# Kernel optimization log

Measured on AMD Instinct MI355X. Metric: run time of the kernel, lower is better.

Reference implementation:

```python
import jax, jax.numpy as jnp
import numpy as np

B, N, F = 1024, 256, 8
E = 1024
OUT = 128          # NNConv out-channels (hardcoded in module)
N_DIV = 64         # len(num_actions)
PER = 3            # actions per diverter
FEAT = N * OUT     # feature_size() = num_nodes * 128


def setup_inputs() -> dict:
    key = jax.random.key(0)
    ks = jax.random.split(key, 20)
    s = lambda *sh: 0.02
    return {
        "x": jax.random.normal(ks[0], (B, N, F), jnp.float32),
        "edge_index": jax.random.randint(ks[1], (2, E), 0, N, jnp.int64),
        # edge-MLP nn1: Linear(1,64) -> ReLU -> Linear(64, F*OUT)
        "w1": jax.random.normal(ks[2], (1, 64), jnp.float32) * 0.1,
        "b1": jnp.zeros((64,), jnp.float32),
        "w2": jax.random.normal(ks[3], (64, F * OUT), jnp.float32) * 0.02,
        "b2": jnp.zeros((F * OUT,), jnp.float32),
        # NNConv root weight + bias
        "root_w": jax.random.normal(ks[4], (F, OUT), jnp.float32) * 0.1,
        "conv_b": jnp.zeros((OUT,), jnp.float32),
        # dueling heads
        "adv_w": jax.random.normal(ks[5], (FEAT, N_DIV * PER), jnp.float32) * 0.005,
        "adv_b": jnp.zeros((N_DIV * PER,), jnp.float32),
        "v1w": jax.random.normal(ks[6], (FEAT, 64), jnp.float32) * 0.005,
        "v1b": jnp.zeros((64,), jnp.float32),
        "v2w": jax.random.normal(ks[7], (64, 64), jnp.float32) * 0.1,
        "v2b": jnp.zeros((64,), jnp.float32),
        "v3w": jax.random.normal(ks[8], (64, N_DIV), jnp.float32) * 0.1,
        "v3b": jnp.zeros((N_DIV,), jnp.float32),
    }


def reference(x, edge_index, w1, b1, w2, b2, root_w, conv_b,
              adv_w, adv_b, v1w, v1b, v2w, v2b, v3w, v3b):
    b, n, f = x.shape
    out_c = root_w.shape[1]
    n_div = v3w.shape[1]
    flat = x.reshape(b * n, f)                              # [B*N, F]
    e = edge_index.shape[1]
    # edge_attr = ones -> edge MLP produces per-edge weight matrix theta
    ea = jnp.ones((e, 1), x.dtype)
    h = jax.nn.relu(ea @ w1 + b1)
    theta = (h @ w2 + b2).reshape(e, f, out_c)              # [E, F, OUT]
    src, tgt = edge_index[0], edge_index[1]
    # gather source feats -> per-edge matmul -> scatter-add at targets
    msg = jnp.einsum('ef,efo->eo', flat[src], theta)        # [E, OUT]
    agg = jnp.zeros((b * n, out_c), x.dtype).at[tgt].add(msg)
    conv = agg + flat @ root_w + conv_b                      # NNConv root + bias
    feat = jax.nn.relu(conv).reshape(b, -1)                  # [B, N*OUT]
    adv = jax.nn.relu(feat @ adv_w + adv_b).reshape(b, n_div, -1)
    val = jax.nn.relu(feat @ v1w + v1b)
    val = jax.nn.relu(val @ v2w + v2b)
    val = val @ v3w + v3b                                    # [B, n_div]
    return val[..., None] + adv - adv.mean(-1, keepdims=True)
```

## Files before the change

kernel.cpp:

```cpp
#include <hip/hip_runtime.h>

#define Bsz 1024
#define Nn 256
#define Fdim 8
#define Eedge 1024
#define OUTC 128
#define CADV 192
#define CTOT 256
#define Ktot 32768
#define ASTR 40
#define XSTR 24

typedef __attribute__((ext_vector_type(8))) short short8;
typedef __attribute__((ext_vector_type(4))) float float4v;

static __device__ inline unsigned short f2bf(float f) {
  union { float f; unsigned u; } v; v.f = f;
  unsigned r = v.u + 0x7FFFu + ((v.u >> 16) & 1u);
  return (unsigned short)(r >> 16);
}
static __device__ inline float bf2f(unsigned short h) {
  union { unsigned u; float f; } v; v.u = ((unsigned)h) << 16;
  return v.f;
}
static __device__ inline uint4 pack8(const unsigned short* b) {
  uint4 v;
  v.x = (unsigned)b[0] | ((unsigned)b[1] << 16);
  v.y = (unsigned)b[2] | ((unsigned)b[3] << 16);
  v.z = (unsigned)b[4] | ((unsigned)b[5] << 16);
  v.w = (unsigned)b[6] | ((unsigned)b[7] << 16);
  return v;
}

__global__ __launch_bounds__(256) void prep_feat_kernel(
    const float* __restrict__ x, const int* __restrict__ ei,
    const float* __restrict__ w1, const float* __restrict__ b1,
    const float* __restrict__ w2, const float* __restrict__ b2,
    const float* __restrict__ rootw, const float* __restrict__ convb,
    const float* __restrict__ advw, const float* __restrict__ v1w,
    unsigned short* __restrict__ wt, unsigned short* __restrict__ feat0)
{
  __shared__ __align__(16) char smem[20480];
  int bid = blockIdx.x, t = threadIdx.x;

  if (bid < 16) {
    float* fs   = (float*)smem;
    float* h_s  = fs;
    float* rw_s = fs + 64;
    float* th_s = fs + 128;
    float* pt_s = fs + 192;
    float* S_s  = fs + 448;
    int*   flag = (int*)(fs + 2496);
    int obase = bid * 8;

    if (t < 64) {
      h_s[t]  = fmaxf(w1[t] + b1[t], 0.f);
      rw_s[t] = rootw[(t >> 3) * OUTC + obase + (t & 7)];
    }
    for (int i = t; i < Nn * Fdim; i += 256) S_s[i] = 0.f;
    if (t == 0) {
      int z = 0;
      for (int i = 1; i < 16; i += 2) z |= ei[i];
      *flag = (z == 0);
    }
    __syncthreads();
    int is64 = *flag;

    {
      int l = t & 63, g = t >> 6;
      int c = (l >> 3) * 128 + obase + (l & 7);
      float p = 0.f;
#pragma unroll
      for (int j = 0; j < 16; ++j)
        p += h_s[g * 16 + j] * w2[(size_t)(g * 16 + j) * 1024 + c];
      pt_s[t] = p;
    }
    int srcs[4], tgts[4];
#pragma unroll
    for (int q = 0; q < 4; ++q) {
      int e = t + q * 256;
      if (is64) { srcs[q] = ei[2 * e]; tgts[q] = ei[2 * (Eedge + e)]; }
      else      { srcs[q] = ei[e];     tgts[q] = ei[Eedge + e]; }
      srcs[q] &= 255; tgts[q] &= 255;
    }
    __syncthreads();
    if (t < 64) {
      int c = (t >> 3) * 128 + obase + (t & 7);
      th_s[t] = b2[c] + pt_s[t] + pt_s[t + 64] + pt_s[t + 128] + pt_s[t + 192];
    }
#pragma unroll
    for (int q = 0; q < 4; ++q) {
      const float* xp = x + srcs[q] * Fdim;
#pragma unroll
      for (int f = 0; f < Fdim; ++f)
        atomicAdd(&S_s[tgts[q] * Fdim + f], xp[f]);
    }
    __syncthreads();
    {
      int n = t;
      const float* xp = x + n * Fdim;
      float4 xa = *(const float4*)xp;
      float4 xb = *(const float4*)(xp + 4);
      float xv[8] = {xa.x, xa.y, xa.z, xa.w, xb.x, xb.y, xb.z, xb.w};
      float sv[8];
#pragma unroll
      for (int f = 0; f < 8; ++f) sv[f] = S_s[n * Fdim + f];
      unsigned short buf[8];
#pragma unroll
      for (int oi = 0; oi < 8; ++oi) {
        float z = convb[obase + oi];
#pragma unroll
        for (int f = 0; f < 8; ++f)
          z += xv[f] * rw_s[f * 8 + oi] + sv[f] * th_s[f * 8 + oi];
        buf[oi] = f2bf(fmaxf(z, 0.f));
      }
      *(uint4*)(feat0 + (size_t)n * OUTC + obase) = pack8(buf);
    }
  } else {
    unsigned short* st = (unsigned short*)smem;
    int kt = bid - 16, c = t;
    const float* src; int stride, col;
    if (c < CADV) { src = advw; stride = CADV; col = c; }
    else          { src = v1w;  stride = 64;   col = c - CADV; }
    float v[32];
#pragma unroll
    for (int i = 0; i < 32; ++i)
      v[i] = src[(size_t)(kt * 32 + i) * stride + col];
    unsigned short bv[32];
#pragma unroll
    for (int i = 0; i < 32; ++i) bv[i] = f2bf(v[i]);
#pragma unroll
    for (int p = 0; p < 4; ++p)
      *(uint4*)(st + c * ASTR + p * 8) = pack8(bv + p * 8);
    __syncthreads();
    uint4* dst = (uint4*)(wt + (size_t)kt * (CTOT * 32));
    for (int r = 0; r < 4; ++r) {
      int s = r * 256 + c;
      dst[s] = *(const uint4*)(st + (s >> 2) * ASTR + (s & 3) * 8);
    }
  }
}

__global__ __launch_bounds__(512, 2) void gemm_mfma(
    const float* __restrict__ x, const unsigned short* __restrict__ wt,
    const float* __restrict__ rootw, const float* __restrict__ convb,
    const unsigned short* __restrict__ feat0, float* __restrict__ part,
    int iters, int ns)
{
  __shared__ short a_s[2][128 * ASTR];
  __shared__ short b_s[2][256 * ASTR];
  __shared__ short x_s[2][128 * XSTR];
  __shared__ short rw_s[128 * XSTR];
  __shared__ float convb_s[128];
  int t = threadIdx.x;
  int ch = blockIdx.x;
  int mb = blockIdx.y;
  int wave = t >> 6, lane = t & 63;
  int wm = wave >> 2, wn = wave & 3;
  int lm = lane & 15, lq = lane >> 4;

  float4v acc[4][4];
#pragma unroll
  for (int i = 0; i < 4; ++i)
#pragma unroll
    for (int j = 0; j < 4; ++j) acc[i][j] = (float4v)0.f;

  int kt0 = ch * iters;
  int iters4 = iters >> 2;
  int n0 = ch * iters4;
  int wr0 = (t >> 2) * ASTR + (t & 3) * 8;
  int u1 = t + 512;
  int wr1 = (u1 >> 2) * ASTR + (u1 & 3) * 8;

  if (t < 128) {
    float wv[8];
#pragma unroll
    for (int f = 0; f < 8; ++f) wv[f] = rootw[f * OUTC + t];
    unsigned short wh[8], wl[8];
#pragma unroll
    for (int f = 0; f < 8; ++f) {
      wh[f] = f2bf(wv[f]);
      wl[f] = f2bf(wv[f] - bf2f(wh[f]));
    }
    *(uint4*)(rw_s + t * XSTR)     = pack8(wh);
    *(uint4*)(rw_s + t * XSTR + 8) = pack8(wl);
    convb_s[t] = convb[t];
  }
  int xr = (t & 255) >> 1, xh = t & 1;
  const float* xgb = x + ((size_t)(mb * 128 + xr) * Nn) * Fdim + xh * 4;
  if (t < 256) {
    float4 xv = *(const float4*)(xgb + (size_t)n0 * Fdim);
    float xa[4] = {xv.x, xv.y, xv.z, xv.w};
    unsigned short hh[4], ll[4];
#pragma unroll
    for (int f = 0; f < 4; ++f) {
      hh[f] = f2bf(xa[f]);
      ll[f] = f2bf(xa[f] - bf2f(hh[f]));
    }
    uint2 dh, dl;
    dh.x = (unsigned)hh[0] | ((unsigned)hh[1] << 16);
    dh.y = (unsigned)hh[2] | ((unsigned)hh[3] << 16);
    dl.x = (unsigned)ll[0] | ((unsigned)ll[1] << 16);
    dl.y = (unsigned)ll[2] | ((unsigned)ll[3] << 16);
    *(uint2*)(x_s[0] + xr * XSTR + xh * 4)     = dh;
    *(uint2*)(x_s[0] + xr * XSTR + 8 + xh * 4) = dl;
  }
  __syncthreads();

  {
    int bloc = wave * 16 + lm;
    short8 xf = (short8)0;
    if (lq == 0 || lq == 2) xf = *(const short8*)(x_s[0] + bloc * XSTR);
    else if (lq == 1)       xf = *(const short8*)(x_s[0] + bloc * XSTR + 8);
#pragma unroll
    for (int tt = 0; tt < 2; ++tt) {
      int ot = tt;
      short8 wf = (short8)0;
      if (lq <= 1)      wf = *(const short8*)(rw_s + (ot * 16 + lm) * XSTR);
      else if (lq == 2) wf = *(const short8*)(rw_s + (ot * 16 + lm) * XSTR + 8);
      float4v c = __builtin_amdgcn_mfma_f32_16x16x32_bf16(wf, xf, (float4v)0.f, 0, 0, 0);
      int o0 = ot * 16 + lq * 4;
      float4 cb = *(const float4*)(convb_s + o0);
      unsigned d0 = (unsigned)f2bf(fmaxf(c[0] + cb.x, 0.f)) |
                    ((unsigned)f2bf(fmaxf(c[1] + cb.y, 0.f)) << 16);
      unsigned d1 = (unsigned)f2bf(fmaxf(c[2] + cb.z, 0.f)) |
                    ((unsigned)f2bf(fmaxf(c[3] + cb.w, 0.f)) << 16);
      if (mb == 0 && bloc == 0) {
        const unsigned* f0p = (const unsigned*)(feat0 + ((size_t)n0 * OUTC + o0));
        d0 = f0p[0]; d1 = f0p[1];
      }
      uint2 dd; dd.x = d0; dd.y = d1;
      *(uint2*)(a_s[0] + bloc * ASTR + tt * 16 + lq * 4) = dd;
    }
  }

  const uint4* gB = (const uint4*)wt + (size_t)kt0 * 1024;
  uint4 vb0 = gB[t], vb1 = gB[t + 512];
  float4 xpf = {0.f, 0.f, 0.f, 0.f};

  for (int kk = 0; kk < iters; ++kk) {
    int g = kk & 3, grp = kk >> 2;
    short* bb = b_s[kk & 1];
    *(uint4*)(bb + wr0) = vb0;
    *(uint4*)(bb + wr1) = vb1;
    if (g == 0 && grp + 1 < iters4 && t < 256)
      xpf = *(const float4*)(xgb + (size_t)(n0 + grp + 1) * Fdim);
    if (g == 3 && grp + 1 < iters4 && t < 256) {
      float xa[4] = {xpf.x, xpf.y, xpf.z, xpf.w};
      unsigned short hh[4], ll[4];
#pragma unroll
      for (int f = 0; f < 4; ++f) {
        hh[f] = f2bf(xa[f]);
        ll[f] = f2bf(xa[f] - bf2f(hh[f]));
      }
      uint2 dh, dl;
      dh.x = (unsigned)hh[0] | ((unsigned)hh[1] << 16);
      dh.y = (unsigned)hh[2] | ((unsigned)hh[3] << 16);
      dl.x = (unsigned)ll[0] | ((unsigned)ll[1] << 16);
      dl.y = (unsigned)ll[2] | ((unsigned)ll[3] << 16);
      short* xd = x_s[(grp + 1) & 1];
      *(uint2*)(xd + xr * XSTR + xh * 4)     = dh;
      *(uint2*)(xd + xr * XSTR + 8 + xh * 4) = dl;
    }
    if (kk + 1 < iters) {
      const uint4* gB2 = (const uint4*)wt + (size_t)(kt0 + kk + 1) * 1024;
      vb0 = gB2[t]; vb1 = gB2[t + 512];
    }
    __syncthreads();

    short* ab = a_s[kk & 1];
    short8 aF[4];
#pragma unroll
    for (int i = 0; i < 4; ++i)
      aF[i] = *(const short8*)(ab + (wm * 64 + i * 16 + lm) * ASTR + lq * 8);
#pragma unroll
    for (int j = 0; j < 4; ++j) {
      short8 bF = *(const short8*)(bb + (wn * 64 + j * 16 + lm) * ASTR + lq * 8);
#pragma unroll
      for (int i = 0; i < 4; ++i)
        acc[i][j] = __builtin_amdgcn_mfma_f32_16x16x32_bf16(bF, aF[i], acc[i][j], 0, 0, 0);
    }

    if (kk + 1 < iters) {
      int kn = kk + 1;
      int g2 = kn & 3, grp2 = kn >> 2;
      const short* xs = x_s[grp2 & 1];
      int node2 = n0 + grp2;
      short* ad = a_s[kn & 1];
      int bloc = wave * 16 + lm;
      short8 xf = (short8)0;
      if (lq == 0 || lq == 2) xf = *(const short8*)(xs + bloc * XSTR);
      else if (lq == 1)       xf = *(const short8*)(xs + bloc * XSTR + 8);
#pragma unroll
      for (int tt = 0; tt < 2; ++tt) {
        int ot = g2 * 2 + tt;
        short8 wf = (short8)0;
        if (lq <= 1)      wf = *(const short8*)(rw_s + (ot * 16 + lm) * XSTR);
        else if (lq == 2) wf = *(const short8*)(rw_s + (ot * 16 + lm) * XSTR + 8);
        float4v c = __builtin_amdgcn_mfma_f32_16x16x32_bf16(wf, xf, (float4v)0.f, 0, 0, 0);
        int o0 = ot * 16 + lq * 4;
        float4 cb = *(const float4*)(convb_s + o0);
        unsigned d0 = (unsigned)f2bf(fmaxf(c[0] + cb.x, 0.f)) |
                      ((unsigned)f2bf(fmaxf(c[1] + cb.y, 0.f)) << 16);
        unsigned d1 = (unsigned)f2bf(fmaxf(c[2] + cb.z, 0.f)) |
                      ((unsigned)f2bf(fmaxf(c[3] + cb.w, 0.f)) << 16);
        if (mb == 0 && bloc == 0) {
          const unsigned* f0p = (const unsigned*)(feat0 + ((size_t)node2 * OUTC + o0));
          d0 = f0p[0]; d1 = f0p[1];
        }
        uint2 dd; dd.x = d0; dd.y = d1;
        *(uint2*)(ad + bloc * ASTR + tt * 16 + lq * 4) = dd;
      }
    }
  }

  float* pb = part + ((size_t)(mb * 128) * ns + ch) * CTOT;
#pragma unroll
  for (int i = 0; i < 4; ++i) {
    int m = wm * 64 + i * 16 + lm;
#pragma unroll
    for (int j = 0; j < 4; ++j) {
      int c = wn * 64 + j * 16 + lq * 4;
      *(float4v*)(pb + (size_t)m * ns * CTOT + c) = acc[i][j];
    }
  }
}

__global__ __launch_bounds__(256) void final_kernel(
    const float* __restrict__ part, int ns,
    const float* __restrict__ advb, const float* __restrict__ v1b,
    const float* __restrict__ v2w, const float* __restrict__ v2b,
    const float* __restrict__ v3w, const float* __restrict__ v3b,
    float* __restrict__ out)
{
  __shared__ float adv_s[CADV];
  __shared__ float v1_s[64];
  __shared__ float val2_s[64];
  __shared__ float val3_s[64];
  int b = blockIdx.x, t = threadIdx.x;
  float s = 0.f;
  const float* p = part + (size_t)b * ns * CTOT + t;
  for (int i = 0; i < ns; ++i) s += p[(size_t)i * CTOT];
  if (t < CADV) adv_s[t] = fmaxf(s + advb[t], 0.f);
  else          v1_s[t - CADV] = fmaxf(s + v1b[t - CADV], 0.f);
  __syncthreads();
  if (t < 64) {
    float a = v2b[t];
#pragma unroll
    for (int i = 0; i < 64; ++i) a += v1_s[i] * v2w[i * 64 + t];
    val2_s[t] = fmaxf(a, 0.f);
  }
  __syncthreads();
  if (t < 64) {
    float a = v3b[t];
#pragma unroll
    for (int j = 0; j < 64; ++j) a += val2_s[j] * v3w[j * 64 + t];
    val3_s[t] = a;
  }
  __syncthreads();
  if (t < CADV) {
    int d = t / 3;
    float mean = (adv_s[d * 3] + adv_s[d * 3 + 1] + adv_s[d * 3 + 2]) * (1.f / 3.f);
    out[(size_t)b * CADV + t] = val3_s[d] + adv_s[t] - mean;
  }
}

extern "C" void kernel_launch(void* const* d_in, const int* in_sizes, int n_in,
                              void* d_out, int out_size, void* d_ws, size_t ws_size,
                              hipStream_t stream)
{
  (void)in_sizes; (void)n_in; (void)out_size;
  const float* x     = (const float*)d_in[0];
  const int*   ei    = (const int*)d_in[1];
  const float* w1    = (const float*)d_in[2];
  const float* b1    = (const float*)d_in[3];
  const float* w2    = (const float*)d_in[4];
  const float* b2    = (const float*)d_in[5];
  const float* rootw = (const float*)d_in[6];
  const float* convb = (const float*)d_in[7];
  const float* advw  = (const float*)d_in[8];
  const float* advb  = (const float*)d_in[9];
  const float* v1w   = (const float*)d_in[10];
  const float* v1b   = (const float*)d_in[11];
  const float* v2w   = (const float*)d_in[12];
  const float* v2b   = (const float*)d_in[13];
  const float* v3w   = (const float*)d_in[14];
  const float* v3b   = (const float*)d_in[15];
  float* out = (float*)d_out;

  const size_t f0B = 131072;
  const size_t wtB = (size_t)Ktot * CTOT * 2;

  int NS = 64;
  while (NS > 8 && f0B + wtB + (size_t)NS * Bsz * CTOT * 4 > ws_size)
    NS >>= 1;

  unsigned short* feat0 = (unsigned short*)d_ws;
  unsigned short* wtp   = (unsigned short*)((char*)d_ws + f0B);
  float* part = (float*)((char*)d_ws + f0B + wtB);

  prep_feat_kernel<<<1040, 256, 0, stream>>>(x, ei, w1, b1, w2, b2, rootw,
                                             convb, advw, v1w, wtp, feat0);
  gemm_mfma<<<dim3(NS, 8), 512, 0, stream>>>(x, wtp, rootw, convb, feat0, part,
                                             1024 / NS, NS);
  final_kernel<<<Bsz, 256, 0, stream>>>(part, NS, advb, v1b, v2w, v2b, v3w, v3b, out);
}
```

Baseline: 173.6 us.

## Pre-swizzle weight tiles into MFMA fragment order and load B directly to registers

The weight pre-transform kernel now writes each K-tile in per-wave MFMA fragment order, so every lane can fetch its B operand straight from global memory into registers. The B shared-memory buffer, its stores and the LDS fragment reads are removed, and the next tile is prefetched into registers after the barrier. This cuts LDS traffic and LDS footprint but makes each wave issue its own global loads, raises register pressure (four extra uint4 prefetch registers), and relies on L2 to serve B reuse across the two waves that share each B slice.

```diff
diff --git a/kernel.cpp b/kernel.cpp
--- a/kernel.cpp
+++ b/kernel.cpp
@@ -135,8 +135,11 @@
     __syncthreads();
     uint4* dst = (uint4*)(wt + (size_t)kt * (CTOT * 32));
     for (int r = 0; r < 4; ++r) {
-      int s = r * 256 + c;
-      dst[s] = *(const uint4*)(st + (s >> 2) * ASTR + (s & 3) * 8);
+      int w = r * 256 + c;
+      int wn = w >> 8, j = (w >> 6) & 3, ln = w & 63;
+      int c2 = wn * 64 + j * 16 + (ln & 15);
+      int ks = ln >> 4;
+      dst[w] = *(const uint4*)(st + c2 * ASTR + ks * 8);
     }
   }
 }
@@ -148,7 +151,6 @@
     int iters, int ns)
 {
   __shared__ short a_s[2][128 * ASTR];
-  __shared__ short b_s[2][256 * ASTR];
   __shared__ short x_s[2][128 * XSTR];
   __shared__ short rw_s[128 * XSTR];
   __shared__ float convb_s[128];
@@ -168,9 +170,7 @@
   int kt0 = ch * iters;
   int iters4 = iters >> 2;
   int n0 = ch * iters4;
-  int wr0 = (t >> 2) * ASTR + (t & 3) * 8;
-  int u1 = t + 512;
-  int wr1 = (u1 >> 2) * ASTR + (u1 & 3) * 8;
+  int boff = wn * 256 + lane;
 
   if (t < 128) {
     float wv[8];
@@ -234,17 +234,16 @@
     }
   }
 
-  const uint4* gB = (const uint4*)wt + (size_t)kt0 * 1024;
-  uint4 vb0 = gB[t], vb1 = gB[t + 512];
+  const uint4* gB = (const uint4*)wt;
+  uint4 vb0, vb1, vb2, vb3;
+  {
+    const uint4* gq = gB + (size_t)kt0 * 1024 + boff;
+    vb0 = gq[0]; vb1 = gq[64]; vb2 = gq[128]; vb3 = gq[192];
+  }
   float4 xpf = {0.f, 0.f, 0.f, 0.f};
 
   for (int kk = 0; kk < iters; ++kk) {
     int g = kk & 3, grp = kk >> 2;
-    short* bb = b_s[kk & 1];
-    *(uint4*)(bb + wr0) = vb0;
-    *(uint4*)(bb + wr1) = vb1;
-    if (g == 0 && grp + 1 < iters4 && t < 256)
-      xpf = *(const float4*)(xgb + (size_t)(n0 + grp + 1) * Fdim);
     if (g == 3 && grp + 1 < iters4 && t < 256) {
       float xa[4] = {xpf.x, xpf.y, xpf.z, xpf.w};
       unsigned short hh[4], ll[4];
@@ -262,26 +261,43 @@
       *(uint2*)(xd + xr * XSTR + xh * 4)     = dh;
       *(uint2*)(xd + xr * XSTR + 8 + xh * 4) = dl;
     }
-    if (kk + 1 < iters) {
-      const uint4* gB2 = (const uint4*)wt + (size_t)(kt0 + kk + 1) * 1024;
-      vb0 = gB2[t]; vb1 = gB2[t + 512];
-    }
     __syncthreads();
+
+    uint4 vbn0, vbn1, vbn2, vbn3;
+    bool pf = (kk + 1 < iters);
+    if (pf) {
+      const uint4* gq = gB + (size_t)(kt0 + kk + 1) * 1024 + boff;
+      vbn0 = gq[0]; vbn1 = gq[64]; vbn2 = gq[128]; vbn3 = gq[192];
+    }
+    if (g == 0 && grp + 1 < iters4 && t < 256)
+      xpf = *(const float4*)(xgb + (size_t)(n0 + grp + 1) * Fdim);
 
     short* ab = a_s[kk & 1];
     short8 aF[4];
 #pragma unroll
     for (int i = 0; i < 4; ++i)
       aF[i] = *(const short8*)(ab + (wm * 64 + i * 16 + lm) * ASTR + lq * 8);
-#pragma unroll
-    for (int j = 0; j < 4; ++j) {
-      short8 bF = *(const short8*)(bb + (wn * 64 + j * 16 + lm) * ASTR + lq * 8);
+    {
+      short8 bF;
+      bF = *(short8*)&vb0;
 #pragma unroll
       for (int i = 0; i < 4; ++i)
-        acc[i][j] = __builtin_amdgcn_mfma_f32_16x16x32_bf16(bF, aF[i], acc[i][j], 0, 0, 0);
-    }
-
-    if (kk + 1 < iters) {
+        acc[i][0] = __builtin_amdgcn_mfma_f32_16x16x32_bf16(bF, aF[i], acc[i][0], 0, 0, 0);
+      bF = *(short8*)&vb1;
+#pragma unroll
+      for (int i = 0; i < 4; ++i)
+        acc[i][1] = __builtin_amdgcn_mfma_f32_16x16x32_bf16(bF, aF[i], acc[i][1], 0, 0, 0);
+      bF = *(short8*)&vb2;
+#pragma unroll
+      for (int i = 0; i < 4; ++i)
+        acc[i][2] = __builtin_amdgcn_mfma_f32_16x16x32_bf16(bF, aF[i], acc[i][2], 0, 0, 0);
+      bF = *(short8*)&vb3;
+#pragma unroll
+      for (int i = 0; i < 4; ++i)
+        acc[i][3] = __builtin_amdgcn_mfma_f32_16x16x32_bf16(bF, aF[i], acc[i][3], 0, 0, 0);
+    }
+
+    if (pf) {
       int kn = kk + 1;
       int g2 = kn & 3, grp2 = kn >> 2;
       const short* xs = x_s[grp2 & 1];
@@ -311,6 +327,7 @@
         uint2 dd; dd.x = d0; dd.y = d1;
         *(uint2*)(ad + bloc * ASTR + tt * 16 + lq * 4) = dd;
       }
+      vb0 = vbn0; vb1 = vbn1; vb2 = vbn2; vb3 = vbn3;
     }
   }
 
```

New measurement: 185.5 us. +6.9%, slower.

## Shrink GEMM M-tile to 32 rows and reduce split-K factor to 16

Applied to the files above, without the earlier changes.

Changes the fused feature-generation GEMM to use 32-row batch tiles instead of 128, with each wave computing one 16-row slice across 64 columns, and launches 32 M-blocks instead of 8. The split-K count drops from 64 to 16, so each block iterates over more K. This is meant to shrink the partial-sum buffer written to and re-read by the final reduction kernel, and to cut register/LDS use per block. In exchange, weight tiles are reused across only 32 rows, so the weight stream is re-read four times as often from L2/HBM, and per-iteration MFMA density falls.

```diff
diff --git a/kernel.cpp b/kernel.cpp
--- a/kernel.cpp
+++ b/kernel.cpp
@@ -147,9 +147,9 @@
     const unsigned short* __restrict__ feat0, float* __restrict__ part,
     int iters, int ns)
 {
-  __shared__ short a_s[2][128 * ASTR];
+  __shared__ short a_s[2][32 * ASTR];
   __shared__ short b_s[2][256 * ASTR];
-  __shared__ short x_s[2][128 * XSTR];
+  __shared__ short x_s[2][32 * XSTR];
   __shared__ short rw_s[128 * XSTR];
   __shared__ float convb_s[128];
   int t = threadIdx.x;
@@ -159,11 +159,9 @@
   int wm = wave >> 2, wn = wave & 3;
   int lm = lane & 15, lq = lane >> 4;
 
-  float4v acc[4][4];
-#pragma unroll
-  for (int i = 0; i < 4; ++i)
-#pragma unroll
-    for (int j = 0; j < 4; ++j) acc[i][j] = (float4v)0.f;
+  float4v acc[4];
+#pragma unroll
+  for (int j = 0; j < 4; ++j) acc[j] = (float4v)0.f;
 
   int kt0 = ch * iters;
   int iters4 = iters >> 2;
@@ -171,6 +169,8 @@
   int wr0 = (t >> 2) * ASTR + (t & 3) * 8;
   int u1 = t + 512;
   int wr1 = (u1 >> 2) * ASTR + (u1 & 3) * 8;
+  int grow = (wave & 1) * 16 + lm;
+  int gtt  = (wave >> 1) & 1;
 
   if (t < 128) {
     float wv[8];
@@ -186,9 +186,9 @@
     *(uint4*)(rw_s + t * XSTR + 8) = pack8(wl);
     convb_s[t] = convb[t];
   }
-  int xr = (t & 255) >> 1, xh = t & 1;
-  const float* xgb = x + ((size_t)(mb * 128 + xr) * Nn) * Fdim + xh * 4;
-  if (t < 256) {
+  int xr = (t & 63) >> 1, xh = t & 1;
+  const float* xgb = x + ((size_t)(mb * 32 + xr) * Nn) * Fdim + xh * 4;
+  if (t < 64) {
     float4 xv = *(const float4*)(xgb + (size_t)n0 * Fdim);
     float xa[4] = {xv.x, xv.y, xv.z, xv.w};
     unsigned short hh[4], ll[4];
@@ -207,31 +207,27 @@
   }
   __syncthreads();
 
-  {
-    int bloc = wave * 16 + lm;
+  if (wave < 4) {
     short8 xf = (short8)0;
-    if (lq == 0 || lq == 2) xf = *(const short8*)(x_s[0] + bloc * XSTR);
-    else if (lq == 1)       xf = *(const short8*)(x_s[0] + bloc * XSTR + 8);
-#pragma unroll
-    for (int tt = 0; tt < 2; ++tt) {
-      int ot = tt;
-      short8 wf = (short8)0;
-      if (lq <= 1)      wf = *(const short8*)(rw_s + (ot * 16 + lm) * XSTR);
-      else if (lq == 2) wf = *(const short8*)(rw_s + (ot * 16 + lm) * XSTR + 8);
-      float4v c = __builtin_amdgcn_mfma_f32_16x16x32_bf16(wf, xf, (float4v)0.f, 0, 0, 0);
-      int o0 = ot * 16 + lq * 4;
-      float4 cb = *(const float4*)(convb_s + o0);
-      unsigned d0 = (unsigned)f2bf(fmaxf(c[0] + cb.x, 0.f)) |
-                    ((unsigned)f2bf(fmaxf(c[1] + cb.y, 0.f)) << 16);
-      unsigned d1 = (unsigned)f2bf(fmaxf(c[2] + cb.z, 0.f)) |
-                    ((unsigned)f2bf(fmaxf(c[3] + cb.w, 0.f)) << 16);
-      if (mb == 0 && bloc == 0) {
-        const unsigned* f0p = (const unsigned*)(feat0 + ((size_t)n0 * OUTC + o0));
-        d0 = f0p[0]; d1 = f0p[1];
-      }
-      uint2 dd; dd.x = d0; dd.y = d1;
-      *(uint2*)(a_s[0] + bloc * ASTR + tt * 16 + lq * 4) = dd;
-    }
+    if (lq == 0 || lq == 2) xf = *(const short8*)(x_s[0] + grow * XSTR);
+    else if (lq == 1)       xf = *(const short8*)(x_s[0] + grow * XSTR + 8);
+    int ot = gtt;
+    short8 wf = (short8)0;
+    if (lq <= 1)      wf = *(const short8*)(rw_s + (ot * 16 + lm) * XSTR);
+    else if (lq == 2) wf = *(const short8*)(rw_s + (ot * 16 + lm) * XSTR + 8);
+    float4v c = __builtin_amdgcn_mfma_f32_16x16x32_bf16(wf, xf, (float4v)0.f, 0, 0, 0);
+    int o0 = ot * 16 + lq * 4;
+    float4 cb = *(const float4*)(convb_s + o0);
+    unsigned d0 = (unsigned)f2bf(fmaxf(c[0] + cb.x, 0.f)) |
+                  ((unsigned)f2bf(fmaxf(c[1] + cb.y, 0.f)) << 16);
+    unsigned d1 = (unsigned)f2bf(fmaxf(c[2] + cb.z, 0.f)) |
+                  ((unsigned)f2bf(fmaxf(c[3] + cb.w, 0.f)) << 16);
+    if (mb == 0 && grow == 0) {
+      const unsigned* f0p = (const unsigned*)(feat0 + ((size_t)n0 * OUTC + o0));
+      d0 = f0p[0]; d1 = f0p[1];
+    }
+    uint2 dd; dd.x = d0; dd.y = d1;
+    *(uint2*)(a_s[0] + grow * ASTR + gtt * 16 + lq * 4) = dd;
   }
 
   const uint4* gB = (const uint4*)wt + (size_t)kt0 * 1024;
@@ -243,9 +239,9 @@
     short* bb = b_s[kk & 1];
     *(uint4*)(bb + wr0) = vb0;
     *(uint4*)(bb + wr1) = vb1;
-    if (g == 0 && grp + 1 < iters4 && t < 256)
+    if (g == 0 && grp + 1 < iters4 && t < 64)
       xpf = *(const float4*)(xgb + (size_t)(n0 + grp + 1) * Fdim);
-    if (g == 3 && grp + 1 < iters4 && t < 256) {
+    if (g == 3 && grp + 1 < iters4 && t < 64) {
       float xa[4] = {xpf.x, xpf.y, xpf.z, xpf.w};
       unsigned short hh[4], ll[4];
 #pragma unroll
@@ -269,60 +265,48 @@
     __syncthreads();
 
     short* ab = a_s[kk & 1];
-    short8 aF[4];
-#pragma unroll
-    for (int i = 0; i < 4; ++i)
-      aF[i] = *(const short8*)(ab + (wm * 64 + i * 16 + lm) * ASTR + lq * 8);
+    short8 aF = *(const short8*)(ab + (wm * 16 + lm) * ASTR + lq * 8);
 #pragma unroll
     for (int j = 0; j < 4; ++j) {
       short8 bF = *(const short8*)(bb + (wn * 64 + j * 16 + lm) * ASTR + lq * 8);
-#pragma unroll
-      for (int i = 0; i < 4; ++i)
-        acc[i][j] = __builtin_amdgcn_mfma_f32_16x16x32_bf16(bF, aF[i], acc[i][j], 0, 0, 0);
-    }
-
-    if (kk + 1 < iters) {
+      acc[j] = __builtin_amdgcn_mfma_f32_16x16x32_bf16(bF, aF, acc[j], 0, 0, 0);
+    }
+
+    if (wave < 4 && kk + 1 < iters) {
       int kn = kk + 1;
       int g2 = kn & 3, grp2 = kn >> 2;
       const short* xs = x_s[grp2 & 1];
       int node2 = n0 + grp2;
       short* ad = a_s[kn & 1];
-      int bloc = wave * 16 + lm;
       short8 xf = (short8)0;
-      if (lq == 0 || lq == 2) xf = *(const short8*)(xs + bloc * XSTR);
-      else if (lq == 1)       xf = *(const short8*)(xs + bloc * XSTR + 8);
-#pragma unroll
-      for (int tt = 0; tt < 2; ++tt) {
-        int ot = g2 * 2 + tt;
-        short8 wf = (short8)0;
-        if (lq <= 1)      wf = *(const short8*)(rw_s + (ot * 16 + lm) * XSTR);
-        else if (lq == 2) wf = *(const short8*)(rw_s + (ot * 16 + lm) * XSTR + 8);
-        float4v c = __builtin_amdgcn_mfma_f32_16x16x32_bf16(wf, xf, (float4v)0.f, 0, 0, 0);
-        int o0 = ot * 16 + lq * 4;
-        float4 cb = *(const float4*)(convb_s + o0);
-        unsigned d0 = (unsigned)f2bf(fmaxf(c[0] + cb.x, 0.f)) |
-                      ((unsigned)f2bf(fmaxf(c[1] + cb.y, 0.f)) << 16);
-        unsigned d1 = (unsigned)f2bf(fmaxf(c[2] + cb.z, 0.f)) |
-                      ((unsigned)f2bf(fmaxf(c[3] + cb.w, 0.f)) << 16);
-        if (mb == 0 && bloc == 0) {
-          const unsigned* f0p = (const unsigned*)(feat0 + ((size_t)node2 * OUTC + o0));
-          d0 = f0p[0]; d1 = f0p[1];
-        }
-        uint2 dd; dd.x = d0; dd.y = d1;
-        *(uint2*)(ad + bloc * ASTR + tt * 16 + lq * 4) = dd;
+      if (lq == 0 || lq == 2) xf = *(const short8*)(xs + grow * XSTR);
+      else if (lq == 1)       xf = *(const short8*)(xs + grow * XSTR + 8);
+      int ot = g2 * 2 + gtt;
+      short8 wf = (short8)0;
+      if (lq <= 1)      wf = *(const short8*)(rw_s + (ot * 16 + lm) * XSTR);
+      else if (lq == 2) wf = *(const short8*)(rw_s + (ot * 16 + lm) * XSTR + 8);
+      float4v c = __builtin_amdgcn_mfma_f32_16x16x32_bf16(wf, xf, (float4v)0.f, 0, 0, 0);
+      int o0 = ot * 16 + lq * 4;
+      float4 cb = *(const float4*)(convb_s + o0);
+      unsigned d0 = (unsigned)f2bf(fmaxf(c[0] + cb.x, 0.f)) |
+                    ((unsigned)f2bf(fmaxf(c[1] + cb.y, 0.f)) << 16);
+      unsigned d1 = (unsigned)f2bf(fmaxf(c[2] + cb.z, 0.f)) |
+                    ((unsigned)f2bf(fmaxf(c[3] + cb.w, 0.f)) << 16);
+      if (mb == 0 && grow == 0) {
+        const unsigned* f0p = (const unsigned*)(feat0 + ((size_t)node2 * OUTC + o0));
+        d0 = f0p[0]; d1 = f0p[1];
       }
-    }
-  }
-
-  float* pb = part + ((size_t)(mb * 128) * ns + ch) * CTOT;
-#pragma unroll
-  for (int i = 0; i < 4; ++i) {
-    int m = wm * 64 + i * 16 + lm;
-#pragma unroll
-    for (int j = 0; j < 4; ++j) {
-      int c = wn * 64 + j * 16 + lq * 4;
-      *(float4v*)(pb + (size_t)m * ns * CTOT + c) = acc[i][j];
-    }
+      uint2 dd; dd.x = d0; dd.y = d1;
+      *(uint2*)(ad + grow * ASTR + gtt * 16 + lq * 4) = dd;
+    }
+  }
+
+  float* pb = part + ((size_t)(mb * 32) * ns + ch) * CTOT;
+#pragma unroll
+  for (int j = 0; j < 4; ++j) {
+    int m = wm * 16 + lm;
+    int c = wn * 64 + j * 16 + lq * 4;
+    *(float4v*)(pb + (size_t)m * ns * CTOT + c) = acc[j];
   }
 }
 
@@ -391,7 +375,7 @@
   const size_t f0B = 131072;
   const size_t wtB = (size_t)Ktot * CTOT * 2;
 
-  int NS = 64;
+  int NS = 16;
   while (NS > 8 && f0B + wtB + (size_t)NS * Bsz * CTOT * 4 > ws_size)
     NS >>= 1;
 
@@ -401,7 +385,7 @@
 
   prep_feat_kernel<<<1040, 256, 0, stream>>>(x, ei, w1, b1, w2, b2, rootw,
                                              convb, advw, v1w, wtp, feat0);
-  gemm_mfma<<<dim3(NS, 8), 512, 0, stream>>>(x, wtp, rootw, convb, feat0, part,
-                                             1024 / NS, NS);
+  gemm_mfma<<<dim3(NS, 32), 512, 0, stream>>>(x, wtp, rootw, convb, feat0, part,
+                                              1024 / NS, NS);
   final_kernel<<<Bsz, 256, 0, stream>>>(part, NS, advb, v1b, v2w, v2b, v3w, v3b, out);
 }
```

Measured after the change: 184.9 us. +6.5%, slower.

## Fuse weight bf16 conversion and node-0 feature prep into the GEMM kernel

Applied to the files above, without the earlier changes.

Removes the separate prep kernel. The GEMM now loads fp32 adv/v1 weights directly with strided loads and converts them to bf16 on the fly, instead of reading a pre-transposed bf16 copy. Blocks with mb==0 compute the edge-aggregated node features for their node range in shared memory. This drops a launch and the extra workspace write/read of the converted weights. In exchange it adds strided uncoalesced fp32 loads, which double the weight read bytes, plus redundant theta/scatter work in each mb==0 block. The workspace-size fallback for NS is also removed.

```diff
diff --git a/kernel.cpp b/kernel.cpp
--- a/kernel.cpp
+++ b/kernel.cpp
@@ -10,6 +10,7 @@
 #define Ktot 32768
 #define ASTR 40
 #define XSTR 24
+#define NSK 64
 
 typedef __attribute__((ext_vector_type(8))) short short8;
 typedef __attribute__((ext_vector_type(4))) float float4v;
@@ -32,126 +33,20 @@
   return v;
 }
 
-__global__ __launch_bounds__(256) void prep_feat_kernel(
-    const float* __restrict__ x, const int* __restrict__ ei,
-    const float* __restrict__ w1, const float* __restrict__ b1,
-    const float* __restrict__ w2, const float* __restrict__ b2,
-    const float* __restrict__ rootw, const float* __restrict__ convb,
-    const float* __restrict__ advw, const float* __restrict__ v1w,
-    unsigned short* __restrict__ wt, unsigned short* __restrict__ feat0)
-{
-  __shared__ __align__(16) char smem[20480];
-  int bid = blockIdx.x, t = threadIdx.x;
-
-  if (bid < 16) {
-    float* fs   = (float*)smem;
-    float* h_s  = fs;
-    float* rw_s = fs + 64;
-    float* th_s = fs + 128;
-    float* pt_s = fs + 192;
-    float* S_s  = fs + 448;
-    int*   flag = (int*)(fs + 2496);
-    int obase = bid * 8;
-
-    if (t < 64) {
-      h_s[t]  = fmaxf(w1[t] + b1[t], 0.f);
-      rw_s[t] = rootw[(t >> 3) * OUTC + obase + (t & 7)];
-    }
-    for (int i = t; i < Nn * Fdim; i += 256) S_s[i] = 0.f;
-    if (t == 0) {
-      int z = 0;
-      for (int i = 1; i < 16; i += 2) z |= ei[i];
-      *flag = (z == 0);
-    }
-    __syncthreads();
-    int is64 = *flag;
-
-    {
-      int l = t & 63, g = t >> 6;
-      int c = (l >> 3) * 128 + obase + (l & 7);
-      float p = 0.f;
-#pragma unroll
-      for (int j = 0; j < 16; ++j)
-        p += h_s[g * 16 + j] * w2[(size_t)(g * 16 + j) * 1024 + c];
-      pt_s[t] = p;
-    }
-    int srcs[4], tgts[4];
-#pragma unroll
-    for (int q = 0; q < 4; ++q) {
-      int e = t + q * 256;
-      if (is64) { srcs[q] = ei[2 * e]; tgts[q] = ei[2 * (Eedge + e)]; }
-      else      { srcs[q] = ei[e];     tgts[q] = ei[Eedge + e]; }
-      srcs[q] &= 255; tgts[q] &= 255;
-    }
-    __syncthreads();
-    if (t < 64) {
-      int c = (t >> 3) * 128 + obase + (t & 7);
-      th_s[t] = b2[c] + pt_s[t] + pt_s[t + 64] + pt_s[t + 128] + pt_s[t + 192];
-    }
-#pragma unroll
-    for (int q = 0; q < 4; ++q) {
-      const float* xp = x + srcs[q] * Fdim;
-#pragma unroll
-      for (int f = 0; f < Fdim; ++f)
-        atomicAdd(&S_s[tgts[q] * Fdim + f], xp[f]);
-    }
-    __syncthreads();
-    {
-      int n = t;
-      const float* xp = x + n * Fdim;
-      float4 xa = *(const float4*)xp;
-      float4 xb = *(const float4*)(xp + 4);
-      float xv[8] = {xa.x, xa.y, xa.z, xa.w, xb.x, xb.y, xb.z, xb.w};
-      float sv[8];
-#pragma unroll
-      for (int f = 0; f < 8; ++f) sv[f] = S_s[n * Fdim + f];
-      unsigned short buf[8];
-#pragma unroll
-      for (int oi = 0; oi < 8; ++oi) {
-        float z = convb[obase + oi];
-#pragma unroll
-        for (int f = 0; f < 8; ++f)
-          z += xv[f] * rw_s[f * 8 + oi] + sv[f] * th_s[f * 8 + oi];
-        buf[oi] = f2bf(fmaxf(z, 0.f));
-      }
-      *(uint4*)(feat0 + (size_t)n * OUTC + obase) = pack8(buf);
-    }
-  } else {
-    unsigned short* st = (unsigned short*)smem;
-    int kt = bid - 16, c = t;
-    const float* src; int stride, col;
-    if (c < CADV) { src = advw; stride = CADV; col = c; }
-    else          { src = v1w;  stride = 64;   col = c - CADV; }
-    float v[32];
-#pragma unroll
-    for (int i = 0; i < 32; ++i)
-      v[i] = src[(size_t)(kt * 32 + i) * stride + col];
-    unsigned short bv[32];
-#pragma unroll
-    for (int i = 0; i < 32; ++i) bv[i] = f2bf(v[i]);
-#pragma unroll
-    for (int p = 0; p < 4; ++p)
-      *(uint4*)(st + c * ASTR + p * 8) = pack8(bv + p * 8);
-    __syncthreads();
-    uint4* dst = (uint4*)(wt + (size_t)kt * (CTOT * 32));
-    for (int r = 0; r < 4; ++r) {
-      int s = r * 256 + c;
-      dst[s] = *(const uint4*)(st + (s >> 2) * ASTR + (s & 3) * 8);
-    }
-  }
-}
-
 __global__ __launch_bounds__(512, 2) void gemm_mfma(
-    const float* __restrict__ x, const unsigned short* __restrict__ wt,
-    const float* __restrict__ rootw, const float* __restrict__ convb,
-    const unsigned short* __restrict__ feat0, float* __restrict__ part,
-    int iters, int ns)
+    const float* __restrict__ x, const float* __restrict__ advw,
+    const float* __restrict__ v1w, const float* __restrict__ rootw,
+    const float* __restrict__ convb, const float* __restrict__ w1,
+    const float* __restrict__ b1, const float* __restrict__ w2,
+    const float* __restrict__ b2, const int* __restrict__ ei,
+    float* __restrict__ part, int iters, int ns)
 {
   __shared__ short a_s[2][128 * ASTR];
   __shared__ short b_s[2][256 * ASTR];
   __shared__ short x_s[2][128 * XSTR];
   __shared__ short rw_s[128 * XSTR];
   __shared__ float convb_s[128];
+  __shared__ unsigned short f0_s[4][128];
   int t = threadIdx.x;
   int ch = blockIdx.x;
   int mb = blockIdx.y;
@@ -171,6 +66,13 @@
   int wr0 = (t >> 2) * ASTR + (t & 3) * 8;
   int u1 = t + 512;
   int wr1 = (u1 >> 2) * ASTR + (u1 & 3) * 8;
+
+  int c2a = t >> 2,        ksa = t & 3;
+  int c2b = u1 >> 2,       ksb = u1 & 3;
+  const float* bsrcA = (c2a < CADV) ? (advw + c2a) : (v1w + (c2a - CADV));
+  int bstrA = (c2a < CADV) ? CADV : 64;
+  const float* bsrcB = (c2b < CADV) ? (advw + c2b) : (v1w + (c2b - CADV));
+  int bstrB = (c2b < CADV) ? CADV : 64;
 
   if (t < 128) {
     float wv[8];
@@ -204,6 +106,57 @@
     dl.y = (unsigned)ll[2] | ((unsigned)ll[3] << 16);
     *(uint2*)(x_s[0] + xr * XSTR + xh * 4)     = dh;
     *(uint2*)(x_s[0] + xr * XSTR + 8 + xh * 4) = dl;
+  }
+
+  if (mb == 0) {
+    float* fs   = (float*)b_s;
+    float* h_s  = fs;
+    float* th_s = fs + 64;
+    float* S_s  = fs + 1088;
+    int*   flag = (int*)(fs + 3136);
+    if (t < 64) h_s[t] = fmaxf(w1[t] + b1[t], 0.f);
+    for (int i = t; i < Nn * Fdim; i += 512) S_s[i] = 0.f;
+    if (t == 0) {
+      int z = 0;
+      for (int i = 1; i < 16; i += 2) z |= ei[i];
+      *flag = (z == 0);
+    }
+    __syncthreads();
+    int is64 = *flag;
+#pragma unroll
+    for (int cc = 0; cc < 2; ++cc) {
+      int c = t + cc * 512;
+      float a2 = b2[c];
+#pragma unroll
+      for (int j = 0; j < 64; ++j) a2 += h_s[j] * w2[(size_t)j * 1024 + c];
+      th_s[c] = a2;
+    }
+    int s0, t0, s1, t1;
+    if (is64) { s0 = ei[2 * t];         t0 = ei[2 * (Eedge + t)];
+                s1 = ei[2 * (t + 512)]; t1 = ei[2 * (Eedge + t + 512)]; }
+    else      { s0 = ei[t];             t0 = ei[Eedge + t];
+                s1 = ei[t + 512];       t1 = ei[Eedge + t + 512]; }
+    s0 &= 255; t0 &= 255; s1 &= 255; t1 &= 255;
+    {
+      const float* xp0 = x + s0 * Fdim;
+      const float* xp1 = x + s1 * Fdim;
+#pragma unroll
+      for (int f = 0; f < Fdim; ++f) {
+        atomicAdd(&S_s[t0 * Fdim + f], xp0[f]);
+        atomicAdd(&S_s[t1 * Fdim + f], xp1[f]);
+      }
+    }
+    __syncthreads();
+    {
+      int nd = t >> 7, o = t & 127, node = n0 + nd;
+      const float* xp = x + node * Fdim;
+      float z = convb[o];
+#pragma unroll
+      for (int f = 0; f < 8; ++f)
+        z += xp[f] * rootw[f * OUTC + o] + S_s[node * Fdim + f] * th_s[f * 128 + o];
+      f0_s[nd][o] = f2bf(fmaxf(z, 0.f));
+    }
+    __syncthreads();
   }
   __syncthreads();
 
@@ -226,7 +179,7 @@
       unsigned d1 = (unsigned)f2bf(fmaxf(c[2] + cb.z, 0.f)) |
                     ((unsigned)f2bf(fmaxf(c[3] + cb.w, 0.f)) << 16);
       if (mb == 0 && bloc == 0) {
-        const unsigned* f0p = (const unsigned*)(feat0 + ((size_t)n0 * OUTC + o0));
+        const unsigned* f0p = (const unsigned*)(&f0_s[0][o0]);
         d0 = f0p[0]; d1 = f0p[1];
       }
       uint2 dd; dd.x = d0; dd.y = d1;
@@ -234,15 +187,25 @@
     }
   }
 
-  const uint4* gB = (const uint4*)wt + (size_t)kt0 * 1024;
-  uint4 vb0 = gB[t], vb1 = gB[t + 512];
+  float rA[8], rB[8];
+  {
+    const float* pa = bsrcA + (size_t)(kt0 * 32 + ksa * 8) * bstrA;
+    const float* pb2 = bsrcB + (size_t)(kt0 * 32 + ksb * 8) * bstrB;
+#pragma unroll
+    for (int i = 0; i < 8; ++i) { rA[i] = pa[i * bstrA]; rB[i] = pb2[i * bstrB]; }
+  }
   float4 xpf = {0.f, 0.f, 0.f, 0.f};
 
   for (int kk = 0; kk < iters; ++kk) {
     int g = kk & 3, grp = kk >> 2;
     short* bb = b_s[kk & 1];
-    *(uint4*)(bb + wr0) = vb0;
-    *(uint4*)(bb + wr1) = vb1;
+    {
+      unsigned short ca[8], cbv[8];
+#pragma unroll
+      for (int i = 0; i < 8; ++i) { ca[i] = f2bf(rA[i]); cbv[i] = f2bf(rB[i]); }
+      *(uint4*)(bb + wr0) = pack8(ca);
+      *(uint4*)(bb + wr1) = pack8(cbv);
+    }
     if (g == 0 && grp + 1 < iters4 && t < 256)
       xpf = *(const float4*)(xgb + (size_t)(n0 + grp + 1) * Fdim);
     if (g == 3 && grp + 1 < iters4 && t < 256) {
@@ -263,8 +226,10 @@
       *(uint2*)(xd + xr * XSTR + 8 + xh * 4) = dl;
     }
     if (kk + 1 < iters) {
-      const uint4* gB2 = (const uint4*)wt + (size_t)(kt0 + kk + 1) * 1024;
-      vb0 = gB2[t]; vb1 = gB2[t + 512];
+      const float* pa = bsrcA + (size_t)((kt0 + kk + 1) * 32 + ksa * 8) * bstrA;
+      const float* pb2 = bsrcB + (size_t)((kt0 + kk + 1) * 32 + ksb * 8) * bstrB;
+#pragma unroll
+      for (int i = 0; i < 8; ++i) { rA[i] = pa[i * bstrA]; rB[i] = pb2[i * bstrB]; }
     }
     __syncthreads();
 
@@ -285,7 +250,6 @@
       int kn = kk + 1;
       int g2 = kn & 3, grp2 = kn >> 2;
       const short* xs = x_s[grp2 & 1];
-      int node2 = n0 + grp2;
       short* ad = a_s[kn & 1];
       int bloc = wave * 16 + lm;
       short8 xf = (short8)0;
@@ -305,7 +269,7 @@
         unsigned d1 = (unsigned)f2bf(fmaxf(c[2] + cb.z, 0.f)) |
                       ((unsigned)f2bf(fmaxf(c[3] + cb.w, 0.f)) << 16);
         if (mb == 0 && bloc == 0) {
-          const unsigned* f0p = (const unsigned*)(feat0 + ((size_t)node2 * OUTC + o0));
+          const unsigned* f0p = (const unsigned*)(&f0_s[grp2][o0]);
           d0 = f0p[0]; d1 = f0p[1];
         }
         uint2 dd; dd.x = d0; dd.y = d1;
@@ -369,7 +333,7 @@
                               void* d_out, int out_size, void* d_ws, size_t ws_size,
                               hipStream_t stream)
 {
-  (void)in_sizes; (void)n_in; (void)out_size;
+  (void)in_sizes; (void)n_in; (void)out_size; (void)ws_size;
   const float* x     = (const float*)d_in[0];
   const int*   ei    = (const int*)d_in[1];
   const float* w1    = (const float*)d_in[2];
@@ -388,20 +352,11 @@
   const float* v3b   = (const float*)d_in[15];
   float* out = (float*)d_out;
 
-  const size_t f0B = 131072;
-  const size_t wtB = (size_t)Ktot * CTOT * 2;
-
-  int NS = 64;
-  while (NS > 8 && f0B + wtB + (size_t)NS * Bsz * CTOT * 4 > ws_size)
-    NS >>= 1;
-
-  unsigned short* feat0 = (unsigned short*)d_ws;
-  unsigned short* wtp   = (unsigned short*)((char*)d_ws + f0B);
-  float* part = (float*)((char*)d_ws + f0B + wtB);
-
-  prep_feat_kernel<<<1040, 256, 0, stream>>>(x, ei, w1, b1, w2, b2, rootw,
-                                             convb, advw, v1w, wtp, feat0);
-  gemm_mfma<<<dim3(NS, 8), 512, 0, stream>>>(x, wtp, rootw, convb, feat0, part,
-                                             1024 / NS, NS);
-  final_kernel<<<Bsz, 256, 0, stream>>>(part, NS, advb, v1b, v2w, v2b, v3w, v3b, out);
-}
+  float* part = (float*)d_ws;
+
+  gemm_mfma<<<dim3(NSK, 8), 512, 0, stream>>>(x, advw, v1w, rootw, convb,
+                                              w1, b1, w2, b2, ei, part,
+                                              1024 / NSK, NSK);
+  final_kernel<<<Bsz, 256, 0, stream>>>(part, NSK, advb, v1b, v2w, v2b, v3w,
+                                        v3b, out);
+}
```

New measurement: 197.3 us. +13.7%, slower.
